# Kernel optimization log

Measured on AMD Instinct MI355X. Metric: run time of the kernel, lower is better.

The kernel has to match this reference:

```python
import jax, jax.numpy as jnp
import numpy as np

HEADS, DIM_HEAD = 8, 64
SCALE = DIM_HEAD ** -0.5
LAMDA1, LAMDA2 = 5.0, 5.0


def setup_inputs() -> dict:
    B, N, M = 32, 1536, 80  # N = 32*48 spatial tokens, M = max_boxes
    QD, KD, VD = 320, 768, 768
    inner = HEADS * DIM_HEAD
    ks = jax.random.split(jax.random.key(0), 11)
    return {
        "x": jax.random.normal(ks[0], (B, N, QD), jnp.float32),
        "key": jax.random.normal(ks[1], (B, M, KD), jnp.float32),
        "value": jax.random.normal(ks[2], (B, M, VD), jnp.float32),
        "mask": jax.random.randint(ks[3], (B, M), 0, 2).astype(bool),
        "perl_box_masking_map": jax.random.normal(ks[4], (B, N, M), jnp.float32),
        "perl_road_masking_map": jax.random.normal(ks[5], (B, 1, N), jnp.float32),
        "Wq": jax.random.normal(ks[6], (inner, QD), jnp.float32) * 0.02,
        "Wk": jax.random.normal(ks[7], (inner, KD), jnp.float32) * 0.02,
        "Wv": jax.random.normal(ks[8], (inner, VD), jnp.float32) * 0.02,
        "Wo": jax.random.normal(ks[9], (QD, inner), jnp.float32) * 0.02,
        "bo": jnp.zeros((QD,), jnp.float32),
    }


def reference(x, key, value, mask, perl_box_masking_map, perl_road_masking_map, Wq, Wk, Wv, Wo, bo):
    B, N, _ = x.shape
    M = key.shape[1]
    H, C = HEADS, DIM_HEAD
    # QKV projections (torch Linear: y = x @ W.T)
    q = (x @ Wq.T).reshape(B, N, H, C)
    k = (key @ Wk.T).reshape(B, M, H, C)
    v = (value @ Wv.T).reshape(B, M, H, C)
    # attention scores with scale, key mask, and two additive bias maps
    sim = jnp.einsum('bnhc,bmhc->bhnm', q, k) * SCALE  # (B, H, N, M)
    neg = -jnp.finfo(sim.dtype).max
    sim = jnp.where(mask[:, None, None, :], sim, neg)  # mask fill BEFORE bias adds, as in torch
    sim = sim + LAMDA1 * perl_box_masking_map[:, None, :, :]
    road = jnp.swapaxes(perl_road_masking_map, 1, 2)  # (B, N, 1) -> broadcast over key axis
    sim = sim + LAMDA2 * road[:, None, :, :]
    attn = jax.nn.softmax(sim, axis=-1)
    out = jnp.einsum('bhnm,bmhc->bnhc', attn, v).reshape(B, N, H * C)
    return out @ Wo.T + bo  # dropout is identity in eval
```

## Files before the change

kernel.cpp:

```cpp
#include <hip/hip_runtime.h>
#include <hip/hip_bf16.h>

typedef __attribute__((ext_vector_type(8))) short short8;
typedef __attribute__((ext_vector_type(4))) short short4v;
typedef __attribute__((ext_vector_type(4))) float floatx4;
typedef __attribute__((ext_vector_type(2))) unsigned uint2v;
typedef unsigned short u16;

#define NB 32
#define NN 1536
#define NM 80
#define NH 8
#define NC 64
#define NINNER 512
#define NQD 320
#define NKD 768

__device__ __forceinline__ float bf2f(u16 u) {
    union { unsigned i; float f; } x; x.i = ((unsigned)u) << 16; return x.f;
}
__device__ __forceinline__ u16 f2bf(float f) {
    unsigned u = __float_as_uint(f);
    unsigned r = (u + 0x7FFFu + ((u >> 16) & 1u)) >> 16;
    return (u16)r;
}
__device__ __forceinline__ unsigned cvt_pk_bf16(float lo, float hi) {
    unsigned r;
    asm("v_cvt_pk_bf16_f32 %0, %1, %2" : "=v"(r) : "v"(lo), "v"(hi));
    return r;
}
__device__ __forceinline__ short8 cvt8(const float* __restrict__ p) {
    float4 a = ((const float4*)p)[0];
    float4 b = ((const float4*)p)[1];
    short8 r;
    r[0] = (short)f2bf(a.x); r[1] = (short)f2bf(a.y);
    r[2] = (short)f2bf(a.z); r[3] = (short)f2bf(a.w);
    r[4] = (short)f2bf(b.x); r[5] = (short)f2bf(b.y);
    r[6] = (short)f2bf(b.z); r[7] = (short)f2bf(b.w);
    return r;
}
__device__ __forceinline__ void gload16(const u16* g, u16* l) {
    __builtin_amdgcn_global_load_lds(
        (const __attribute__((address_space(1))) unsigned int*)g,
        (__attribute__((address_space(3))) unsigned int*)l, 16, 0, 0);
}

__global__ __launch_bounds__(256) void prep(const u16* __restrict__ x,
                                            const unsigned char* __restrict__ raw,
                                            int* __restrict__ flag,
                                            float* __restrict__ maskbias) {
    if (blockIdx.x == 0) {
        __shared__ int cnt;
        if (threadIdx.x == 0) cnt = 0;
        __syncthreads();
        int c = 0;
        for (int i = threadIdx.x; i < 8192; i += 256) {
            unsigned e = (x[i] >> 7) & 0xFF;
            if (e >= 0xA0) c++;
        }
        atomicAdd(&cnt, c);
        __syncthreads();
        if (threadIdx.x == 0) *flag = (cnt > 64) ? 1 : 0;
    } else {
        __shared__ int c_bf, c_f32, c_u8;
        if (threadIdx.x == 0) { c_bf = 0; c_f32 = 0; c_u8 = 0; }
        __syncthreads();
        for (int i = threadIdx.x; i < NB * NM; i += 256) {
            unsigned char v = raw[i];
            if (v == 0x3F && (i & 3) == 1) atomicAdd(&c_bf, 1);
            if (v == 0x3F && (i & 3) == 3) atomicAdd(&c_f32, 1);
            if (v != 0 && (i & 3) != 0) atomicAdd(&c_u8, 1);
        }
        __syncthreads();
        int md;
        if (c_bf > 0) md = 2;
        else if (c_f32 > 0) md = 3;
        else if (c_u8 > 0) md = 1;
        else md = 0;
        for (int i = threadIdx.x; i < NB * NM; i += 256) {
            bool on;
            if (md == 2) on = ((const u16*)raw)[i] != 0;
            else if (md == 3) on = ((const float*)raw)[i] != 0.0f;
            else if (md == 1) on = raw[i] != 0;
            else on = ((const int*)raw)[i] != 0;
            maskbias[i] = on ? 0.0f : -3.4028234663852886e38f;
        }
    }
}

struct ConvSeg { const void* src; u16* dst; long nreal; long nblk; };
struct ConvArgs { ConvSeg s[7]; };

__global__ __launch_bounds__(256) void conv_batch(ConvArgs a, const int* __restrict__ flag) {
    const int f = *flag;
    long b = blockIdx.x; int seg = 0;
    while (seg < 7 && b >= a.s[seg].nblk) { b -= a.s[seg].nblk; seg++; }
    if (seg >= 7) return;
    const long idx = b * 2048 + threadIdx.x * 8;
    u16* dst = a.s[seg].dst;
    if (idx >= a.s[seg].nreal) { *(short8*)(dst + idx) = (short8)0; return; }
    if (f) *(short8*)(dst + idx) = cvt8((const float*)a.s[seg].src + idx);
    else   *(short8*)(dst + idx) = *(const short8*)((const u16*)a.s[seg].src + idx);
}

template <bool OUT_DYN, bool BIAS>
__device__ __forceinline__ void gemm_body(const u16* __restrict__ A,
                                          const u16* __restrict__ B,
                                          const void* __restrict__ bias,
                                          void* __restrict__ C,
                                          int bx, int by, int Nreal, int K, int f,
                                          u16* As, u16* Bs) {
    const int tid = threadIdx.x;
    const int wave = tid >> 6, lane = tid & 63;
    const int l16 = lane & 15, quad = lane >> 4;
    const int wr = wave >> 1, wc = wave & 1;
    const int bm0 = bx * 128, bn0 = by * 128;

    const int r0 = tid >> 2, c0 = tid & 3;
    const int sc = c0 ^ ((r0 >> 1) & 3);
    const u16* Ag = A + (size_t)(bm0 + r0) * K + sc * 8;
    const u16* Bg = B + (size_t)(bn0 + r0) * K + sc * 8;

    const int swz = (l16 >> 1) & 3;
    floatx4 acc[4][4];
#pragma unroll
    for (int i = 0; i < 4; ++i)
#pragma unroll
        for (int n = 0; n < 4; ++n) acc[i][n] = (floatx4)0.0f;

    {
        u16* AsW = As + wave * 512;
        u16* BsW = Bs + wave * 512;
        gload16(Ag, AsW);                  gload16(Ag + (size_t)64 * K, AsW + 2048);
        gload16(Bg, BsW);                  gload16(Bg + (size_t)64 * K, BsW + 2048);
    }
    __syncthreads();

    int cur = 0;
    for (int kk = 0; kk < K; kk += 32) {
        if (kk + 32 < K) {
            u16* AsW = As + (cur ^ 1) * 4096 + wave * 512;
            u16* BsW = Bs + (cur ^ 1) * 4096 + wave * 512;
            gload16(Ag + kk + 32, AsW);
            gload16(Ag + (size_t)64 * K + kk + 32, AsW + 2048);
            gload16(Bg + kk + 32, BsW);
            gload16(Bg + (size_t)64 * K + kk + 32, BsW + 2048);
        }
        const u16* Asr = As + cur * 4096;
        const u16* Bsr = Bs + cur * 4096;
        short8 af[4], bf[4];
#pragma unroll
        for (int i = 0; i < 4; ++i)
            af[i] = *(const short8*)&Asr[(wr * 64 + i * 16 + l16) * 32 + ((quad ^ swz) * 8)];
#pragma unroll
        for (int n = 0; n < 4; ++n)
            bf[n] = *(const short8*)&Bsr[(wc * 64 + n * 16 + l16) * 32 + ((quad ^ swz) * 8)];
#pragma unroll
        for (int i = 0; i < 4; ++i)
#pragma unroll
            for (int n = 0; n < 4; ++n)
                acc[i][n] = __builtin_amdgcn_mfma_f32_16x16x32_bf16(af[i], bf[n], acc[i][n], 0, 0, 0);
        __syncthreads();
        cur ^= 1;
    }

#pragma unroll
    for (int n = 0; n < 4; ++n) {
        const int col = bn0 + wc * 64 + n * 16 + l16;
        if (col < Nreal) {
            float badd = 0.0f;
            if (BIAS) badd = f ? ((const float*)bias)[col] : bf2f(((const u16*)bias)[col]);
#pragma unroll
            for (int i = 0; i < 4; ++i)
#pragma unroll
                for (int r = 0; r < 4; ++r) {
                    const int row = bm0 + wr * 64 + i * 16 + quad * 4 + r;
                    const float val = acc[i][n][r] + badd;
                    if (OUT_DYN && f) ((float*)C)[(size_t)row * Nreal + col] = val;
                    else              ((u16*)C)[(size_t)row * Nreal + col] = f2bf(val);
                }
        }
    }
}

struct GemmRoles {
    const u16* A[3]; const u16* B[3]; u16* C[3];
    int mblk[3]; int kdim[3]; int start[3];
};

__global__ __launch_bounds__(256) void gemm_qkv(GemmRoles g) {
    __shared__ __align__(16) u16 As[2 * 128 * 32];
    __shared__ __align__(16) u16 Bs[2 * 128 * 32];
    const int id = blockIdx.x;
    const int role = (id >= g.start[1]) + (id >= g.start[2]);
    const int rid = id - g.start[role];
    const int mb = g.mblk[role];
    const int bx = rid % mb, by = rid / mb;
    gemm_body<false, false>(g.A[role], g.B[role], nullptr, g.C[role],
                            bx, by, NINNER, g.kdim[role], 0, As, Bs);
}

__global__ __launch_bounds__(256) void gemm_out(const u16* __restrict__ A,
                                                const u16* __restrict__ B,
                                                const void* __restrict__ bias,
                                                void* __restrict__ C,
                                                const int* __restrict__ flag) {
    __shared__ __align__(16) u16 As[2 * 128 * 32];
    __shared__ __align__(16) u16 Bs[2 * 128 * 32];
    const int f = *flag;
    gemm_body<true, true>(A, B, bias, C, blockIdx.x, blockIdx.y, NQD, NINNER, f, As, Bs);
}

__global__ __launch_bounds__(256) void transpose_v(const u16* __restrict__ v,
                                                   u16* __restrict__ vT) {
    int b = blockIdx.x >> 3, h = blockIdx.x & 7;
    const u16* src = v + (size_t)b * NM * NINNER + h * NC;
    u16* o = vT + (size_t)(b * NH + h) * NC * 96;
    for (int idx = threadIdx.x; idx < NM * NC; idx += 256) {
        int m = idx >> 6, c = idx & 63;
        o[c * 96 + m] = src[(size_t)m * NINNER + c];
    }
    for (int idx = threadIdx.x; idx < NC * 16; idx += 256) {
        int c = idx >> 4, m = 80 + (idx & 15);
        o[c * 96 + m] = 0;
    }
}

__global__ __launch_bounds__(256) void attn_kernel(const u16* __restrict__ q,
                                                   const u16* __restrict__ k,
                                                   const u16* __restrict__ vT,
                                                   const float* __restrict__ maskbias,
                                                   const void* __restrict__ box,
                                                   const void* __restrict__ road,
                                                   u16* __restrict__ attno,
                                                   const int* __restrict__ flag) {
    const int f = *flag;
    const int n0 = blockIdx.x * 64;
    const int h = blockIdx.y;
    const int b = blockIdx.z;
    const int tid = threadIdx.x;
    const int wave = tid >> 6, lane = tid & 63;
    const int l16 = lane & 15, quad = lane >> 4;

    __shared__ __align__(16) u16 p_lds[64][104];

    const int n = n0 + 16 * wave + l16;
    const size_t qrow = (size_t)(b * NN + n) * NINNER + h * NC;
    short8 qa[2];
    qa[0] = *(const short8*)(q + qrow + 0 + quad * 8);
    qa[1] = *(const short8*)(q + qrow + 32 + quad * 8);
    short8 kf[5][2];
#pragma unroll
    for (int mt = 0; mt < 5; ++mt) {
        const u16* kr = k + (size_t)(b * NM + mt * 16 + l16) * NINNER + h * NC + quad * 8;
        kf[mt][0] = *(const short8*)(kr + 0);
        kf[mt][1] = *(const short8*)(kr + 32);
    }
    const size_t boxbase = ((size_t)b * NN + n) * NM;
    floatx4 bx4[5]; short4v bxh[5]; floatx4 mb4[5];
    float roadf = 0.0f; u16 roadh = 0;
    if (f) {
#pragma unroll
        for (int mt = 0; mt < 5; ++mt)
            bx4[mt] = *(const floatx4*)((const float*)box + boxbase + 16 * mt + 4 * quad);
        roadf = ((const float*)road)[(size_t)b * NN + n];
    } else {
#pragma unroll
        for (int mt = 0; mt < 5; ++mt)
            bxh[mt] = *(const short4v*)((const u16*)box + boxbase + 16 * mt + 4 * quad);
        roadh = ((const u16*)road)[(size_t)b * NN + n];
    }
#pragma unroll
    for (int mt = 0; mt < 5; ++mt)
        mb4[mt] = *(const floatx4*)(maskbias + b * NM + 16 * mt + 4 * quad);

    floatx4 s[5];
#pragma unroll
    for (int i = 0; i < 5; ++i) s[i] = (floatx4)0.0f;
#pragma unroll
    for (int kk2 = 0; kk2 < 2; ++kk2)
#pragma unroll
        for (int mt = 0; mt < 5; ++mt)
            s[mt] = __builtin_amdgcn_mfma_f32_16x16x32_bf16(kf[mt][kk2], qa[kk2], s[mt], 0, 0, 0);

    const u16* vbase = vT + (size_t)(b * NH + h) * NC * 96;
    short8 vf[3][4];
#pragma unroll
    for (int kt = 0; kt < 3; ++kt)
#pragma unroll
        for (int nt = 0; nt < 4; ++nt)
            vf[kt][nt] = *(const short8*)(vbase + (size_t)(nt * 16 + l16) * 96 + kt * 32 + quad * 8);

    const float roadv = 5.0f * (f ? roadf : bf2f(roadh));
    floatx4 cb[5];
#pragma unroll
    for (int mt = 0; mt < 5; ++mt)
#pragma unroll
        for (int r = 0; r < 4; ++r) {
            const float boxv = f ? bx4[mt][r] : bf2f((u16)bxh[mt][r]);
            cb[mt][r] = mb4[mt][r] + 5.0f * boxv + roadv;
        }

#pragma unroll
    for (int mt = 0; mt < 5; ++mt)
#pragma unroll
        for (int r = 0; r < 4; ++r)
            s[mt][r] = s[mt][r] * 0.125f + cb[mt][r];

    float mx;
    {
        float t0 = fmaxf(fmaxf(s[0][0], s[0][1]), fmaxf(s[0][2], s[0][3]));
        float t1 = fmaxf(fmaxf(s[1][0], s[1][1]), fmaxf(s[1][2], s[1][3]));
        float t2 = fmaxf(fmaxf(s[2][0], s[2][1]), fmaxf(s[2][2], s[2][3]));
        float t3 = fmaxf(fmaxf(s[3][0], s[3][1]), fmaxf(s[3][2], s[3][3]));
        float t4 = fmaxf(fmaxf(s[4][0], s[4][1]), fmaxf(s[4][2], s[4][3]));
        mx = fmaxf(fmaxf(fmaxf(t0, t1), fmaxf(t2, t3)), t4);
    }
    mx = fmaxf(mx, __shfl_xor(mx, 16));
    mx = fmaxf(mx, __shfl_xor(mx, 32));
    float sum = 0.0f;
#pragma unroll
    for (int mt = 0; mt < 5; ++mt)
#pragma unroll
        for (int r = 0; r < 4; ++r) {
            const float p = __expf(s[mt][r] - mx);
            s[mt][r] = p;
            sum += p;
        }
    sum += __shfl_xor(sum, 16);
    sum += __shfl_xor(sum, 32);
    const float inv = 1.0f / sum;

#pragma unroll
    for (int mt = 0; mt < 5; ++mt) {
        uint2v pk;
        pk[0] = cvt_pk_bf16(s[mt][0] * inv, s[mt][1] * inv);
        pk[1] = cvt_pk_bf16(s[mt][2] * inv, s[mt][3] * inv);
        *(uint2v*)&p_lds[16 * wave + l16][16 * mt + 4 * quad] = pk;
    }
    if (quad < 2) *(short8*)&p_lds[16 * wave + l16][80 + 8 * quad] = (short8)0;
    asm volatile("s_waitcnt lgkmcnt(0)" ::: "memory");
    __builtin_amdgcn_sched_barrier(0);

    floatx4 o[4];
#pragma unroll
    for (int i = 0; i < 4; ++i) o[i] = (floatx4)0.0f;
#pragma unroll
    for (int kt = 0; kt < 3; ++kt) {
        short8 a = *(const short8*)&p_lds[16 * wave + l16][kt * 32 + quad * 8];
#pragma unroll
        for (int nt = 0; nt < 4; ++nt)
            o[nt] = __builtin_amdgcn_mfma_f32_16x16x32_bf16(a, vf[kt][nt], o[nt], 0, 0, 0);
    }

#pragma unroll
    for (int nt = 0; nt < 4; ++nt) {
#pragma unroll
        for (int r = 0; r < 4; ++r) {
            int nr = n0 + 16 * wave + quad * 4 + r;
            attno[((size_t)b * NN + nr) * NINNER + h * NC + nt * 16 + l16] = f2bf(o[nt][r]);
        }
    }
}

extern "C" void kernel_launch(void* const* d_in, const int* in_sizes, int n_in,
                              void* d_out, int out_size, void* d_ws, size_t ws_size,
                              hipStream_t stream) {
    (void)in_sizes; (void)n_in; (void)out_size; (void)ws_size;
    const void* x    = d_in[0];
    const void* key  = d_in[1];
    const void* val  = d_in[2];
    const unsigned char* mask = (const unsigned char*)d_in[3];
    const void* box  = d_in[4];
    const void* road = d_in[5];
    const void* Wq   = d_in[6];
    const void* Wk   = d_in[7];
    const void* Wv   = d_in[8];
    const void* Wo   = d_in[9];
    const void* bo   = d_in[10];

    char* ws = (char*)d_ws;
    size_t off = 0;
    auto carve = [&](size_t bytes) {
        char* p = ws + off;
        off += (bytes + 255) & ~(size_t)255;
        return p;
    };
    int* flag   = (int*)carve(256);
    u16* q_ws   = (u16*)carve((size_t)NB * NN * NINNER * 2);
    u16* k_ws   = (u16*)carve((size_t)NB * NM * NINNER * 2);
    u16* v_ws   = (u16*)carve((size_t)NB * NM * NINNER * 2);
    u16* vT_ws  = (u16*)carve((size_t)NB * NH * NC * 96 * 2);
    u16* ao_ws  = (u16*)carve((size_t)NB * NN * NINNER * 2);
    u16* x_bf   = ao_ws;
    u16* key_bf = (u16*)carve((size_t)NB * NM * NKD * 2);
    u16* val_bf = (u16*)carve((size_t)NB * NM * NKD * 2);
    u16* Wq_bf  = (u16*)carve((size_t)NINNER * NQD * 2);
    u16* Wk_bf  = (u16*)carve((size_t)NINNER * NKD * 2);
    u16* Wv_bf  = (u16*)carve((size_t)NINNER * NKD * 2);
    u16* WoP_bf = (u16*)carve((size_t)384 * NINNER * 2);
    float* mb   = (float*)carve((size_t)NB * NM * 4);

    prep<<<2, 256, 0, stream>>>((const u16*)x, mask, flag, mb);

    ConvArgs ca;
    ca.s[0] = { x,     x_bf,   (long)NB * NN * NQD, (long)NB * NN * NQD / 2048 };
    ca.s[1] = { key,   key_bf, (long)NB * NM * NKD, (long)NB * NM * NKD / 2048 };
    ca.s[2] = { val,   val_bf, (long)NB * NM * NKD, (long)NB * NM * NKD / 2048 };
    ca.s[3] = { Wq,    Wq_bf,  (long)NINNER * NQD,  (long)NINNER * NQD / 2048 };
    ca.s[4] = { Wk,    Wk_bf,  (long)NINNER * NKD,  (long)NINNER * NKD / 2048 };
    ca.s[5] = { Wv,    Wv_bf,  (long)NINNER * NKD,  (long)NINNER * NKD / 2048 };
    ca.s[6] = { Wo,    WoP_bf, (long)NQD * NINNER,  (long)384 * NINNER / 2048 };
    long totblk = 0;
    for (int i = 0; i < 7; ++i) totblk += ca.s[i].nblk;
    conv_batch<<<(int)totblk, 256, 0, stream>>>(ca, flag);

    GemmRoles g;
    g.A[0] = key_bf; g.B[0] = Wk_bf; g.C[0] = k_ws; g.mblk[0] = NB * NM / 128; g.kdim[0] = NKD;
    g.A[1] = val_bf; g.B[1] = Wv_bf; g.C[1] = v_ws; g.mblk[1] = NB * NM / 128; g.kdim[1] = NKD;
    g.A[2] = x_bf;   g.B[2] = Wq_bf; g.C[2] = q_ws; g.mblk[2] = NB * NN / 128; g.kdim[2] = NQD;
    g.start[0] = 0;
    g.start[1] = g.mblk[0] * 4;
    g.start[2] = g.start[1] + g.mblk[1] * 4;
    int gtot = g.start[2] + g.mblk[2] * 4;
    gemm_qkv<<<gtot, 256, 0, stream>>>(g);

    transpose_v<<<NB * NH, 256, 0, stream>>>(v_ws, vT_ws);
    attn_kernel<<<dim3(NN / 64, NH, NB), 256, 0, stream>>>(
        q_ws, k_ws, vT_ws, mb, box, road, ao_ws, flag);
    gemm_out<<<dim3(NB * NN / 128, 384 / 128), 256, 0, stream>>>(
        ao_ws, WoP_bf, bo, d_out, flag);
}
```

Baseline: 324.8 us.

## Stage K and V tiles in swizzled LDS via async global loads in attention

The attention kernel previously had every lane load its own K and V MFMA fragments straight from global memory into registers. Each block now stages the head's whole K tile and a transposed V tile in LDS using 16-byte direct-to-LDS global loads. It then reads the fragments from LDS with an XOR swizzle meant to avoid bank conflicts. The V transpose kernel now pads to 128 columns and writes the swizzled layout. This cuts redundant global traffic and register pressure, at the cost of a block barrier, extra LDS per block (which may lower occupancy) and a larger vT buffer.

```diff
diff --git a/kernel.cpp b/kernel.cpp
--- a/kernel.cpp
+++ b/kernel.cpp
@@ -215,14 +215,11 @@
                                                    u16* __restrict__ vT) {
     int b = blockIdx.x >> 3, h = blockIdx.x & 7;
     const u16* src = v + (size_t)b * NM * NINNER + h * NC;
-    u16* o = vT + (size_t)(b * NH + h) * NC * 96;
-    for (int idx = threadIdx.x; idx < NM * NC; idx += 256) {
-        int m = idx >> 6, c = idx & 63;
-        o[c * 96 + m] = src[(size_t)m * NINNER + c];
-    }
-    for (int idx = threadIdx.x; idx < NC * 16; idx += 256) {
-        int c = idx >> 4, m = 80 + (idx & 15);
-        o[c * 96 + m] = 0;
+    u16* o = vT + (size_t)(b * NH + h) * NC * 128;
+    for (int idx = threadIdx.x; idx < NC * 128; idx += 256) {
+        int c = idx >> 7, m = idx & 127;
+        u16 val = (m < NM) ? src[(size_t)m * NINNER + c] : (u16)0;
+        o[c * 128 + ((((m >> 3) ^ (c & 7))) << 3) + (m & 7)] = val;
     }
 }
 
@@ -242,20 +239,33 @@
     const int wave = tid >> 6, lane = tid & 63;
     const int l16 = lane & 15, quad = lane >> 4;
 
+    __shared__ __align__(16) u16 K_lds[80 * 64];
+    __shared__ __align__(16) u16 V_lds[64 * 128];
     __shared__ __align__(16) u16 p_lds[64][104];
+
+    {
+        const int row0 = tid >> 3;
+        const int cswz = (tid & 7) ^ (row0 & 7);
+        const u16* kg = k + ((size_t)b * NM + row0) * NINNER + h * NC + cswz * 8;
+        u16* kw = K_lds + wave * 512;
+        gload16(kg, kw);
+        gload16(kg + (size_t)32 * NINNER, kw + 2048);
+        if (wave < 2)
+            gload16(kg + (size_t)64 * NINNER, kw + 4096);
+    }
+    {
+        const u16* vg = vT + (size_t)(b * NH + h) * NC * 128 + tid * 8;
+        u16* vw = V_lds + wave * 512;
+#pragma unroll
+        for (int i = 0; i < 4; ++i)
+            gload16(vg + i * 2048, vw + i * 2048);
+    }
 
     const int n = n0 + 16 * wave + l16;
     const size_t qrow = (size_t)(b * NN + n) * NINNER + h * NC;
     short8 qa[2];
     qa[0] = *(const short8*)(q + qrow + 0 + quad * 8);
     qa[1] = *(const short8*)(q + qrow + 32 + quad * 8);
-    short8 kf[5][2];
-#pragma unroll
-    for (int mt = 0; mt < 5; ++mt) {
-        const u16* kr = k + (size_t)(b * NM + mt * 16 + l16) * NINNER + h * NC + quad * 8;
-        kf[mt][0] = *(const short8*)(kr + 0);
-        kf[mt][1] = *(const short8*)(kr + 32);
-    }
     const size_t boxbase = ((size_t)b * NN + n) * NM;
     floatx4 bx4[5]; short4v bxh[5]; floatx4 mb4[5];
     float roadf = 0.0f; u16 roadh = 0;
@@ -274,23 +284,6 @@
     for (int mt = 0; mt < 5; ++mt)
         mb4[mt] = *(const floatx4*)(maskbias + b * NM + 16 * mt + 4 * quad);
 
-    floatx4 s[5];
-#pragma unroll
-    for (int i = 0; i < 5; ++i) s[i] = (floatx4)0.0f;
-#pragma unroll
-    for (int kk2 = 0; kk2 < 2; ++kk2)
-#pragma unroll
-        for (int mt = 0; mt < 5; ++mt)
-            s[mt] = __builtin_amdgcn_mfma_f32_16x16x32_bf16(kf[mt][kk2], qa[kk2], s[mt], 0, 0, 0);
-
-    const u16* vbase = vT + (size_t)(b * NH + h) * NC * 96;
-    short8 vf[3][4];
-#pragma unroll
-    for (int kt = 0; kt < 3; ++kt)
-#pragma unroll
-        for (int nt = 0; nt < 4; ++nt)
-            vf[kt][nt] = *(const short8*)(vbase + (size_t)(nt * 16 + l16) * 96 + kt * 32 + quad * 8);
-
     const float roadv = 5.0f * (f ? roadf : bf2f(roadh));
     floatx4 cb[5];
 #pragma unroll
@@ -299,6 +292,20 @@
         for (int r = 0; r < 4; ++r) {
             const float boxv = f ? bx4[mt][r] : bf2f((u16)bxh[mt][r]);
             cb[mt][r] = mb4[mt][r] + 5.0f * boxv + roadv;
+        }
+
+    __syncthreads();
+
+    const int rsw = l16 & 7;
+    floatx4 s[5];
+#pragma unroll
+    for (int i = 0; i < 5; ++i) s[i] = (floatx4)0.0f;
+#pragma unroll
+    for (int kk2 = 0; kk2 < 2; ++kk2)
+#pragma unroll
+        for (int mt = 0; mt < 5; ++mt) {
+            short8 kfr = *(const short8*)&K_lds[(mt * 16 + l16) * 64 + (((kk2 * 4 + quad) ^ rsw) * 8)];
+            s[mt] = __builtin_amdgcn_mfma_f32_16x16x32_bf16(kfr, qa[kk2], s[mt], 0, 0, 0);
         }
 
 #pragma unroll
@@ -347,10 +354,12 @@
     for (int i = 0; i < 4; ++i) o[i] = (floatx4)0.0f;
 #pragma unroll
     for (int kt = 0; kt < 3; ++kt) {
-        short8 a = *(const short8*)&p_lds[16 * wave + l16][kt * 32 + quad * 8];
-#pragma unroll
-        for (int nt = 0; nt < 4; ++nt)
-            o[nt] = __builtin_amdgcn_mfma_f32_16x16x32_bf16(a, vf[kt][nt], o[nt], 0, 0, 0);
+        short8 pb = *(const short8*)&p_lds[16 * wave + l16][kt * 32 + quad * 8];
+#pragma unroll
+        for (int nt = 0; nt < 4; ++nt) {
+            short8 vfr = *(const short8*)&V_lds[(nt * 16 + l16) * 128 + (((kt * 4 + quad) ^ rsw) * 8)];
+            o[nt] = __builtin_amdgcn_mfma_f32_16x16x32_bf16(pb, vfr, o[nt], 0, 0, 0);
+        }
     }
 
 #pragma unroll
@@ -390,7 +399,7 @@
     u16* q_ws   = (u16*)carve((size_t)NB * NN * NINNER * 2);
     u16* k_ws   = (u16*)carve((size_t)NB * NM * NINNER * 2);
     u16* v_ws   = (u16*)carve((size_t)NB * NM * NINNER * 2);
-    u16* vT_ws  = (u16*)carve((size_t)NB * NH * NC * 96 * 2);
+    u16* vT_ws  = (u16*)carve((size_t)NB * NH * NC * 128 * 2);
     u16* ao_ws  = (u16*)carve((size_t)NB * NN * NINNER * 2);
     u16* x_bf   = ao_ws;
     u16* key_bf = (u16*)carve((size_t)NB * NM * NKD * 2);
```

After: 298.1 us. 1.09x faster.
